# Kernel tuning notes

Hardware: AMD Instinct MI355X
Metric: run time of the kernel (lower is better)

## Reference

```python
import jax, jax.numpy as jnp
import numpy as np

EPS = 1e-7


def setup_inputs() -> dict:
    key = jax.random.key(0)
    k1, k2, k3, k4 = jax.random.split(key, 4)
    S, N, R, CIN, COUT = 16, 1024, 4, 128, 128
    A = jax.random.uniform(k1, (S, N, N, R + 1), dtype=jnp.float32)
    x = jax.random.normal(k2, (S, N, CIN), dtype=jnp.float32)
    weight = jax.random.normal(k3, (CIN, COUT, R), dtype=jnp.float32) * 0.02
    theta_root = jax.random.normal(k4, (CIN, COUT), dtype=jnp.float32) * 0.02
    return {"A": A, "x": x, "weight": weight, "theta_root": theta_root}


def reference(A, x, weight, theta_root):
    # Drop the last relation channel ('no-edge' type in MolGAN)
    Ar = A[..., :-1]                                   # (s, N, N, R)
    # Per-destination, per-relation degree normalization
    norm = 1.0 / (jnp.sum(Ar, axis=2) + EPS)           # (s, N, R)
    # Fused contraction: avoid materializing Theta_ij (s,N,N,in,out).
    # x_new[s,i,b] = sum_{j,c,a} A[s,i,j,c] * norm[s,i,c] * x[s,j,a] * W[a,b,c]
    m = jnp.einsum('sijc,sja->sica', Ar, x)            # (s, N, R, in)
    m = m * norm[..., None]                            # apply norm over (s,i,c)
    agg = jnp.einsum('sica,abc->sib', m, weight)       # (s, N, out)
    x_new = agg + x @ theta_root                       # root/self term
    return jnp.tanh(x_new)
```

## Files before the change

kernel.cpp:

```cpp
#include <hip/hip_runtime.h>
#include <hip/hip_bf16.h>
#include <math.h>

#define SS   16
#define NN   1024
#define RR   4
#define CINC 128
#define COUTC 128
#define RP1  5
#define EPSF 1e-7f

typedef __bf16 bf16x8 __attribute__((ext_vector_type(8)));
typedef __bf16 bf16x4 __attribute__((ext_vector_type(4)));
typedef float  f32x4  __attribute__((ext_vector_type(4)));

#define YT_BYTES ((size_t)SS * RR * COUTC * NN * 2)

__global__ __launch_bounds__(256) void prep_kernel(
    const float* __restrict__ x, const float* __restrict__ weight,
    const float* __restrict__ theta, __bf16* __restrict__ Yt,
    float* __restrict__ Z)
{
    const int bx = blockIdx.x;
    const int it = bx & 15;
    const int ch = (bx >> 4) % 5;
    const int s  = (bx >> 4) / 5;

    __shared__ __bf16 lx[64 * 136];
    __shared__ __bf16 lw[128 * 136];

    const int t = threadIdx.x;
    {
        const int i = t >> 2, q = t & 3;
        const float* xrow = x + ((size_t)s * NN + it * 64 + i) * CINC;
#pragma unroll
        for (int k = 0; k < 8; ++k) {
            f32x4 v = *(const f32x4*)(xrow + q * 32 + k * 4);
            bf16x4 b; b[0] = (__bf16)v.x; b[1] = (__bf16)v.y; b[2] = (__bf16)v.z; b[3] = (__bf16)v.w;
            *(bf16x4*)&lx[i * 136 + q * 32 + k * 4] = b;
        }
    }
    {
        const int b = t >> 1, h = t & 1;
        if (ch < 4) {
#pragma unroll
            for (int k = 0; k < 64; ++k) {
                const int a = h * 64 + k;
                lw[b * 136 + a] = (__bf16)weight[(a * COUTC + b) * RR + ch];
            }
        } else {
#pragma unroll
            for (int k = 0; k < 64; ++k) {
                const int a = h * 64 + k;
                lw[b * 136 + a] = (__bf16)theta[a * COUTC + b];
            }
        }
    }
    __syncthreads();

    const int lane = t & 63, w = t >> 6;
    const int m16 = lane & 15, quad = lane >> 4;

    f32x4 acc[8];
#pragma unroll
    for (int i = 0; i < 8; ++i) acc[i] = (f32x4){0.f, 0.f, 0.f, 0.f};

#pragma unroll
    for (int k0 = 0; k0 < CINC; k0 += 32) {
        const bf16x8 af = *(const bf16x8*)&lx[(w * 16 + m16) * 136 + k0 + quad * 8];
#pragma unroll
        for (int bs = 0; bs < 8; ++bs) {
            const bf16x8 bf = *(const bf16x8*)&lw[(bs * 16 + m16) * 136 + k0 + quad * 8];
            acc[bs] = __builtin_amdgcn_mfma_f32_16x16x32_bf16(af, bf, acc[bs], 0, 0, 0);
        }
    }

    const int j0 = it * 64 + w * 16 + quad * 4;
    if (ch < 4) {
#pragma unroll
        for (int bs = 0; bs < 8; ++bs) {
            const int b = bs * 16 + m16;
            __bf16* p = Yt + (((size_t)(s * 4 + ch) * COUTC + b) * NN + j0);
            bf16x4 v; v[0] = (__bf16)acc[bs][0]; v[1] = (__bf16)acc[bs][1];
                      v[2] = (__bf16)acc[bs][2]; v[3] = (__bf16)acc[bs][3];
            *(bf16x4*)p = v;
        }
    } else {
#pragma unroll
        for (int bs = 0; bs < 8; ++bs) {
            const int b = bs * 16 + m16;
#pragma unroll
            for (int r = 0; r < 4; ++r)
                Z[((size_t)s * NN + j0 + r) * COUTC + b] = acc[bs][r];
        }
    }
}

__global__ __launch_bounds__(256, 2) void main_kernel(
    const float* __restrict__ A, const __bf16* __restrict__ Yt,
    const float* __restrict__ Z, float* __restrict__ out)
{
    const int bx = blockIdx.x;
    const int s  = bx >> 5;
    const int i0 = (bx & 31) * 32;

    __shared__ __bf16 lA[4][32][40];
    __shared__ float  lnorm[4][32];

    const int t = threadIdx.x;
    const int lane = t & 63, w = t >> 6;
    const int m16 = lane & 15, quad = lane >> 4;

    const int irow = t >> 3;
    const int q    = t & 7;

    const float* Ap = A + ((size_t)(s * NN + i0 + irow) * NN) * RP1 + q * 20;

    float rs[4] = {0.f, 0.f, 0.f, 0.f};
    f32x4 acc[4][2][2];
#pragma unroll
    for (int c = 0; c < 4; ++c)
#pragma unroll
        for (int is = 0; is < 2; ++is)
#pragma unroll
            for (int bs = 0; bs < 2; ++bs) acc[c][is][bs] = (f32x4){0.f, 0.f, 0.f, 0.f};

    const __bf16* Ys = Yt + (size_t)s * 4 * COUTC * NN;

    f32x4 ld[5];
#pragma unroll
    for (int u = 0; u < 5; ++u) ld[u] = __builtin_nontemporal_load((const f32x4*)Ap + u);

    for (int kk = 0; kk < 32; ++kk) {
        bf16x8 bf[4][2];
        const __bf16* yp = Ys + kk * 32 + quad * 8;
#pragma unroll
        for (int c = 0; c < 4; ++c)
#pragma unroll
            for (int bs = 0; bs < 2; ++bs)
                bf[c][bs] = *(const bf16x8*)(yp + (size_t)(c * COUTC + w * 32 + bs * 16 + m16) * NN);

        __syncthreads();

        {
            const float v0[4] = {ld[0].x, ld[1].y, ld[2].z, ld[3].w};
            const float v1[4] = {ld[0].y, ld[1].z, ld[2].w, ld[4].x};
            const float v2[4] = {ld[0].z, ld[1].w, ld[3].x, ld[4].y};
            const float v3[4] = {ld[0].w, ld[2].x, ld[3].y, ld[4].z};
            const float* vv[4] = {v0, v1, v2, v3};
#pragma unroll
            for (int c = 0; c < 4; ++c) {
                const float* v = vv[c];
                rs[c] += v[0] + v[1] + v[2] + v[3];
                bf16x4 pk; pk[0] = (__bf16)v[0]; pk[1] = (__bf16)v[1];
                           pk[2] = (__bf16)v[2]; pk[3] = (__bf16)v[3];
                *(bf16x4*)&lA[c][irow][q * 4] = pk;
            }
        }
        __syncthreads();

        if (kk < 31) {
            Ap += 160;
#pragma unroll
            for (int u = 0; u < 5; ++u) ld[u] = __builtin_nontemporal_load((const f32x4*)Ap + u);
        }

#pragma unroll
        for (int c = 0; c < 4; ++c) {
            const bf16x8 af0 = *(const bf16x8*)&lA[c][m16][quad * 8];
            const bf16x8 af1 = *(const bf16x8*)&lA[c][16 + m16][quad * 8];
            acc[c][0][0] = __builtin_amdgcn_mfma_f32_16x16x32_bf16(af0, bf[c][0], acc[c][0][0], 0, 0, 0);
            acc[c][0][1] = __builtin_amdgcn_mfma_f32_16x16x32_bf16(af0, bf[c][1], acc[c][0][1], 0, 0, 0);
            acc[c][1][0] = __builtin_amdgcn_mfma_f32_16x16x32_bf16(af1, bf[c][0], acc[c][1][0], 0, 0, 0);
            acc[c][1][1] = __builtin_amdgcn_mfma_f32_16x16x32_bf16(af1, bf[c][1], acc[c][1][1], 0, 0, 0);
        }
    }

#pragma unroll
    for (int c = 0; c < 4; ++c) {
        float v = rs[c];
        v += __shfl_xor(v, 1);
        v += __shfl_xor(v, 2);
        v += __shfl_xor(v, 4);
        if (q == 0) lnorm[c][irow] = 1.0f / (v + EPSF);
    }
    __syncthreads();

#pragma unroll
    for (int is = 0; is < 2; ++is) {
        f32x4 nv[4];
#pragma unroll
        for (int c = 0; c < 4; ++c) nv[c] = *(const f32x4*)&lnorm[c][is * 16 + quad * 4];
        const int row0 = i0 + is * 16 + quad * 4;
#pragma unroll
        for (int bs = 0; bs < 2; ++bs) {
            const int b = w * 32 + bs * 16 + m16;
#pragma unroll
            for (int r = 0; r < 4; ++r) {
                float v = acc[0][is][bs][r] * nv[0][r]
                        + acc[1][is][bs][r] * nv[1][r]
                        + acc[2][is][bs][r] * nv[2][r]
                        + acc[3][is][bs][r] * nv[3][r];
                const size_t idx = ((size_t)s * NN + row0 + r) * COUTC + b;
                out[idx] = tanhf(v + Z[idx]);
            }
        }
    }
}

extern "C" void kernel_launch(void* const* d_in, const int* in_sizes, int n_in,
                              void* d_out, int out_size, void* d_ws, size_t ws_size,
                              hipStream_t stream)
{
    const float* A      = (const float*)d_in[0];
    const float* x      = (const float*)d_in[1];
    const float* weight = (const float*)d_in[2];
    const float* theta  = (const float*)d_in[3];
    float* out = (float*)d_out;

    __bf16* Yt = (__bf16*)d_ws;
    float*  Z  = (float*)((char*)d_ws + YT_BYTES);

    prep_kernel<<<dim3(SS * 5 * 16), dim3(256), 0, stream>>>(x, weight, theta, Yt, Z);
    main_kernel<<<dim3(SS * 32), dim3(256), 0, stream>>>(A, Yt, Z, out);
}
```

Baseline: 567.8 us.

## Pre-convert inputs to bf16, double-buffer A tile, and reorder block mapping

Adds a conversion kernel that casts x to bf16 once and transposes the weights and theta into a bf16 layout. The prep kernel then reads MFMA operands straight from global memory and no longer stages them through LDS with strided weight reads. In the main kernel the LDS tile for A is double-buffered, which drops one barrier per iteration, and the Y fragment loads move after the barrier. Blocks are interleaved across samples so that consecutive blocks touch different samples. The cost is an extra kernel launch and extra workspace traffic.

```diff
diff --git a/kernel.cpp b/kernel.cpp
--- a/kernel.cpp
+++ b/kernel.cpp
@@ -2,96 +2,93 @@
 #include <hip/hip_bf16.h>
 #include <math.h>
 
-#define SS   16
-#define NN   1024
-#define RR   4
-#define CINC 128
+#define SS    16
+#define NN    1024
+#define RR    4
+#define CINC  128
 #define COUTC 128
-#define RP1  5
-#define EPSF 1e-7f
+#define RP1   5
+#define EPSF  1e-7f
 
 typedef __bf16 bf16x8 __attribute__((ext_vector_type(8)));
 typedef __bf16 bf16x4 __attribute__((ext_vector_type(4)));
 typedef float  f32x4  __attribute__((ext_vector_type(4)));
 
 #define YT_BYTES ((size_t)SS * RR * COUTC * NN * 2)
+#define Z_BYTES  ((size_t)SS * NN * COUTC * 4)
+#define XB_BYTES ((size_t)SS * NN * CINC * 2)
+
+__global__ __launch_bounds__(256) void convert_kernel(
+    const float* __restrict__ x, const float* __restrict__ weight,
+    const float* __restrict__ theta, __bf16* __restrict__ xb,
+    __bf16* __restrict__ wT)
+{
+    const int bx = blockIdx.x, t = threadIdx.x;
+    if (bx < 1024) {
+        const size_t e0 = ((size_t)bx * 256 + t) * 8;
+        f32x4 v0 = *(const f32x4*)(x + e0);
+        f32x4 v1 = *(const f32x4*)(x + e0 + 4);
+        bf16x8 o;
+        o[0] = (__bf16)v0.x; o[1] = (__bf16)v0.y; o[2] = (__bf16)v0.z; o[3] = (__bf16)v0.w;
+        o[4] = (__bf16)v1.x; o[5] = (__bf16)v1.y; o[6] = (__bf16)v1.z; o[7] = (__bf16)v1.w;
+        *(bf16x8*)(xb + e0) = o;
+    } else if (t < 128) {
+        const int a = bx - 1024;
+        f32x4 wv = *(const f32x4*)(weight + ((size_t)a * COUTC + t) * RR);
+        wT[(0 * COUTC + t) * CINC + a] = (__bf16)wv.x;
+        wT[(1 * COUTC + t) * CINC + a] = (__bf16)wv.y;
+        wT[(2 * COUTC + t) * CINC + a] = (__bf16)wv.z;
+        wT[(3 * COUTC + t) * CINC + a] = (__bf16)wv.w;
+        wT[(4 * COUTC + t) * CINC + a] = (__bf16)theta[(size_t)a * COUTC + t];
+    }
+}
 
 __global__ __launch_bounds__(256) void prep_kernel(
-    const float* __restrict__ x, const float* __restrict__ weight,
-    const float* __restrict__ theta, __bf16* __restrict__ Yt,
-    float* __restrict__ Z)
+    const __bf16* __restrict__ xb, const __bf16* __restrict__ wT,
+    __bf16* __restrict__ Yt, float* __restrict__ Z)
 {
     const int bx = blockIdx.x;
-    const int it = bx & 15;
-    const int ch = (bx >> 4) % 5;
-    const int s  = (bx >> 4) / 5;
-
-    __shared__ __bf16 lx[64 * 136];
-    __shared__ __bf16 lw[128 * 136];
-
-    const int t = threadIdx.x;
-    {
-        const int i = t >> 2, q = t & 3;
-        const float* xrow = x + ((size_t)s * NN + it * 64 + i) * CINC;
-#pragma unroll
-        for (int k = 0; k < 8; ++k) {
-            f32x4 v = *(const f32x4*)(xrow + q * 32 + k * 4);
-            bf16x4 b; b[0] = (__bf16)v.x; b[1] = (__bf16)v.y; b[2] = (__bf16)v.z; b[3] = (__bf16)v.w;
-            *(bf16x4*)&lx[i * 136 + q * 32 + k * 4] = b;
-        }
-    }
-    {
-        const int b = t >> 1, h = t & 1;
-        if (ch < 4) {
-#pragma unroll
-            for (int k = 0; k < 64; ++k) {
-                const int a = h * 64 + k;
-                lw[b * 136 + a] = (__bf16)weight[(a * COUTC + b) * RR + ch];
-            }
-        } else {
-#pragma unroll
-            for (int k = 0; k < 64; ++k) {
-                const int a = h * 64 + k;
-                lw[b * 136 + a] = (__bf16)theta[a * COUTC + b];
-            }
-        }
-    }
-    __syncthreads();
-
-    const int lane = t & 63, w = t >> 6;
+    const int s  = bx & 15;
+    const int r  = bx >> 4;
+    const int ch = r % 5;
+    const int jt = r / 5;
+
+    const int t = threadIdx.x, lane = t & 63, w = t >> 6;
     const int m16 = lane & 15, quad = lane >> 4;
 
+    const __bf16* xrow = xb + ((size_t)(s * NN) + jt * 64 + w * 16 + m16) * CINC;
+    const __bf16* wch  = wT + (size_t)ch * COUTC * CINC;
+
     f32x4 acc[8];
 #pragma unroll
     for (int i = 0; i < 8; ++i) acc[i] = (f32x4){0.f, 0.f, 0.f, 0.f};
 
 #pragma unroll
     for (int k0 = 0; k0 < CINC; k0 += 32) {
-        const bf16x8 af = *(const bf16x8*)&lx[(w * 16 + m16) * 136 + k0 + quad * 8];
+        const bf16x8 af = *(const bf16x8*)(xrow + k0 + quad * 8);
 #pragma unroll
         for (int bs = 0; bs < 8; ++bs) {
-            const bf16x8 bf = *(const bf16x8*)&lw[(bs * 16 + m16) * 136 + k0 + quad * 8];
+            const bf16x8 bf = *(const bf16x8*)(wch + (size_t)(bs * 16 + m16) * CINC + k0 + quad * 8);
             acc[bs] = __builtin_amdgcn_mfma_f32_16x16x32_bf16(af, bf, acc[bs], 0, 0, 0);
         }
     }
 
-    const int j0 = it * 64 + w * 16 + quad * 4;
+    const int j0 = jt * 64 + w * 16 + quad * 4;
     if (ch < 4) {
 #pragma unroll
         for (int bs = 0; bs < 8; ++bs) {
             const int b = bs * 16 + m16;
-            __bf16* p = Yt + (((size_t)(s * 4 + ch) * COUTC + b) * NN + j0);
             bf16x4 v; v[0] = (__bf16)acc[bs][0]; v[1] = (__bf16)acc[bs][1];
                       v[2] = (__bf16)acc[bs][2]; v[3] = (__bf16)acc[bs][3];
-            *(bf16x4*)p = v;
+            *(bf16x4*)(Yt + ((size_t)((s * 4 + ch) * COUTC + b)) * NN + j0) = v;
         }
     } else {
 #pragma unroll
         for (int bs = 0; bs < 8; ++bs) {
             const int b = bs * 16 + m16;
 #pragma unroll
-            for (int r = 0; r < 4; ++r)
-                Z[((size_t)s * NN + j0 + r) * COUTC + b] = acc[bs][r];
+            for (int r4 = 0; r4 < 4; ++r4)
+                Z[((size_t)s * NN + j0 + r4) * COUTC + b] = acc[bs][r4];
         }
     }
 }
@@ -101,10 +98,10 @@
     const float* __restrict__ Z, float* __restrict__ out)
 {
     const int bx = blockIdx.x;
-    const int s  = bx >> 5;
-    const int i0 = (bx & 31) * 32;
-
-    __shared__ __bf16 lA[4][32][40];
+    const int s  = bx & 15;
+    const int i0 = (bx >> 4) * 32;
+
+    __shared__ __bf16 lA[2][4][32][40];
     __shared__ float  lnorm[4][32];
 
     const int t = threadIdx.x;
@@ -132,15 +129,7 @@
     for (int u = 0; u < 5; ++u) ld[u] = __builtin_nontemporal_load((const f32x4*)Ap + u);
 
     for (int kk = 0; kk < 32; ++kk) {
-        bf16x8 bf[4][2];
-        const __bf16* yp = Ys + kk * 32 + quad * 8;
-#pragma unroll
-        for (int c = 0; c < 4; ++c)
-#pragma unroll
-            for (int bs = 0; bs < 2; ++bs)
-                bf[c][bs] = *(const bf16x8*)(yp + (size_t)(c * COUTC + w * 32 + bs * 16 + m16) * NN);
-
-        __syncthreads();
+        const int p = kk & 1;
 
         {
             const float v0[4] = {ld[0].x, ld[1].y, ld[2].z, ld[3].w};
@@ -154,7 +143,7 @@
                 rs[c] += v[0] + v[1] + v[2] + v[3];
                 bf16x4 pk; pk[0] = (__bf16)v[0]; pk[1] = (__bf16)v[1];
                            pk[2] = (__bf16)v[2]; pk[3] = (__bf16)v[3];
-                *(bf16x4*)&lA[c][irow][q * 4] = pk;
+                *(bf16x4*)&lA[p][c][irow][q * 4] = pk;
             }
         }
         __syncthreads();
@@ -165,10 +154,18 @@
             for (int u = 0; u < 5; ++u) ld[u] = __builtin_nontemporal_load((const f32x4*)Ap + u);
         }
 
+        bf16x8 bf[4][2];
+        const __bf16* yp = Ys + kk * 32 + quad * 8;
+#pragma unroll
+        for (int c = 0; c < 4; ++c)
+#pragma unroll
+            for (int bs = 0; bs < 2; ++bs)
+                bf[c][bs] = *(const bf16x8*)(yp + (size_t)(c * COUTC + w * 32 + bs * 16 + m16) * NN);
+
 #pragma unroll
         for (int c = 0; c < 4; ++c) {
-            const bf16x8 af0 = *(const bf16x8*)&lA[c][m16][quad * 8];
-            const bf16x8 af1 = *(const bf16x8*)&lA[c][16 + m16][quad * 8];
+            const bf16x8 af0 = *(const bf16x8*)&lA[p][c][m16][quad * 8];
+            const bf16x8 af1 = *(const bf16x8*)&lA[p][c][16 + m16][quad * 8];
             acc[c][0][0] = __builtin_amdgcn_mfma_f32_16x16x32_bf16(af0, bf[c][0], acc[c][0][0], 0, 0, 0);
             acc[c][0][1] = __builtin_amdgcn_mfma_f32_16x16x32_bf16(af0, bf[c][1], acc[c][0][1], 0, 0, 0);
             acc[c][1][0] = __builtin_amdgcn_mfma_f32_16x16x32_bf16(af1, bf[c][0], acc[c][1][0], 0, 0, 0);
@@ -220,7 +217,10 @@
 
     __bf16* Yt = (__bf16*)d_ws;
     float*  Z  = (float*)((char*)d_ws + YT_BYTES);
-
-    prep_kernel<<<dim3(SS * 5 * 16), dim3(256), 0, stream>>>(x, weight, theta, Yt, Z);
+    __bf16* xb = (__bf16*)((char*)d_ws + YT_BYTES + Z_BYTES);
+    __bf16* wT = (__bf16*)((char*)d_ws + YT_BYTES + Z_BYTES + XB_BYTES);
+
+    convert_kernel<<<dim3(1024 + 128), dim3(256), 0, stream>>>(x, weight, theta, xb, wT);
+    prep_kernel<<<dim3(SS * 5 * 16), dim3(256), 0, stream>>>(xb, wT, Yt, Z);
     main_kernel<<<dim3(SS * 32), dim3(256), 0, stream>>>(A, Yt, Z, out);
 }
```

Measured after the change: 585.9 us. +3.2%, slower.
